# Kernel optimization log

Measured on AMD Instinct MI355X. Metric: run time of the kernel, lower is better.

## Reference

```python
import jax, jax.numpy as jnp
import numpy as np


def setup_inputs() -> dict:
    key = jax.random.key(0)
    ks = jax.random.split(key, 8)
    T, D = 8192, 36
    return {
        "embeddings": jax.random.normal(ks[0], (T, D), dtype=jnp.float32),
        "WQ_prog": jax.random.normal(ks[1], (2, D), dtype=jnp.float32),
        "WK_prog": jax.random.normal(ks[2], (2, D), dtype=jnp.float32),
        "WV_op": jax.random.normal(ks[3], (1, D), dtype=jnp.float32),
        "WV_arg": jax.random.normal(ks[4], (1, D), dtype=jnp.float32),
        "WQ_stack": jax.random.normal(ks[5], (2, D), dtype=jnp.float32),
        "WK_stack": jax.random.normal(ks[6], (2, D), dtype=jnp.float32),
        "WV_stack": jax.random.normal(ks[7], (1, D), dtype=jnp.float32),
    }


def reference(embeddings, WQ_prog, WK_prog, WV_op, WV_arg, WQ_stack, WK_stack, WV_stack):
    # --- program-fetch head: hard-argmax attention ---
    Q_prog = embeddings @ WQ_prog.T          # (T, 2)
    K_prog = embeddings @ WK_prog.T          # (T, 2)
    V_op = embeddings @ WV_op.T              # (T, 1)
    V_arg = embeddings @ WV_arg.T            # (T, 1)
    scores_prog = Q_prog @ K_prog.T          # (T, T)
    best_prog = jnp.argmax(scores_prog, axis=1)   # (T,)
    fetched_ops = V_op[best_prog, 0]
    fetched_args = V_arg[best_prog, 0]

    # --- stack-fetch head: hard-argmax attention ---
    Q_stack = embeddings @ WQ_stack.T        # (T, 2)
    K_stack = embeddings @ WK_stack.T        # (T, 2)
    V_stack = embeddings @ WV_stack.T        # (T, 1)
    scores_stack = Q_stack @ K_stack.T       # (T, T)
    best_stack = jnp.argmax(scores_stack, axis=1)
    fetched_vals = V_stack[best_stack, 0]

    return (fetched_ops, fetched_args, fetched_vals)
```

## Files before the change

### kernel.cpp

```cpp
#include <hip/hip_runtime.h>
#include <math.h>

#define T 8192
#define D 36
#define NCH 8
#define CHUNK (T / NCH)


__global__ __launch_bounds__(256) void proj_kernel(
    const float* __restrict__ E,
    const float* __restrict__ WQp, const float* __restrict__ WKp,
    const float* __restrict__ WVop, const float* __restrict__ WVarg,
    const float* __restrict__ WQs, const float* __restrict__ WKs,
    const float* __restrict__ WVs, float* __restrict__ ws) {
    int t = blockIdx.x * blockDim.x + threadIdx.x;
    if (t >= T) return;
    float e[D];
    const float4* Er = (const float4*)(E + t * D);
#pragma unroll
    for (int i = 0; i < D / 4; ++i) {
        float4 v = Er[i];
        e[4 * i + 0] = v.x; e[4 * i + 1] = v.y;
        e[4 * i + 2] = v.z; e[4 * i + 3] = v.w;
    }
    float qp0 = 0.f, qp1 = 0.f, kp0 = 0.f, kp1 = 0.f;
    float qs0 = 0.f, qs1 = 0.f, ks0 = 0.f, ks1 = 0.f;
    float vop = 0.f, varg = 0.f, vs = 0.f;
#pragma unroll
    for (int d = 0; d < D; ++d) {
        float ed = e[d];
        qp0 = fmaf(ed, WQp[d], qp0);
        qp1 = fmaf(ed, WQp[D + d], qp1);
        kp0 = fmaf(ed, WKp[d], kp0);
        kp1 = fmaf(ed, WKp[D + d], kp1);
        qs0 = fmaf(ed, WQs[d], qs0);
        qs1 = fmaf(ed, WQs[D + d], qs1);
        ks0 = fmaf(ed, WKs[d], ks0);
        ks1 = fmaf(ed, WKs[D + d], ks1);
        vop  = fmaf(ed, WVop[d], vop);
        varg = fmaf(ed, WVarg[d], varg);
        vs   = fmaf(ed, WVs[d], vs);
    }
    ws[t]          = qp0;
    ws[T + t]      = qp1;
    ws[2 * T + 2 * t]     = kp0;
    ws[2 * T + 2 * t + 1] = kp1;
    ws[4 * T + t]  = qs0;
    ws[5 * T + t]  = qs1;
    ws[6 * T + 2 * t]     = ks0;
    ws[6 * T + 2 * t + 1] = ks1;
    ws[8 * T + t]  = vop;
    ws[9 * T + t]  = varg;
    ws[10 * T + t] = vs;
}

__global__ __launch_bounds__(256) void argmax_kernel(
    const float* __restrict__ wsf, float* __restrict__ pv, int* __restrict__ pi) {
    const int head = blockIdx.z;
    const float* Q0 = wsf + (head ? 4 * T : 0);
    const float* Q1 = Q0 + T;
    const float2* K = (const float2*)(wsf + (head ? 6 * T : 2 * T));

    __shared__ float2 sk[CHUNK];
    const int j0 = blockIdx.y * CHUNK;
    for (int k = threadIdx.x; k < CHUNK; k += 256) sk[k] = K[j0 + k];
    __syncthreads();

    const int row = blockIdx.x * 256 + threadIdx.x;
    const float q0 = Q0[row], q1 = Q1[row];
    float best = -INFINITY;
    int bi = 0;
#pragma unroll 8
    for (int k = 0; k < CHUNK; ++k) {
        float2 kk = sk[k];
        float s = fmaf(q0, kk.x, q1 * kk.y);
        bool gt = s > best;
        best = gt ? s : best;
        bi   = gt ? k : bi;
    }
    const int prow = head * T + row;
    pv[prow * NCH + blockIdx.y] = best;
    pi[prow * NCH + blockIdx.y] = j0 + bi;
}

__global__ __launch_bounds__(256) void finalize_kernel(
    const float* __restrict__ wsf, const float* __restrict__ pv,
    const int* __restrict__ pi, float* __restrict__ out) {
    int idx = blockIdx.x * blockDim.x + threadIdx.x;
    if (idx >= 2 * T) return;
    const int head = idx >> 13;
    const int row  = idx & (T - 1);
    float best = -INFINITY;
    int bi = 0;
#pragma unroll
    for (int c = 0; c < NCH; ++c) {
        float v = pv[idx * NCH + c];
        int   i2 = pi[idx * NCH + c];
        bool gt = v > best;
        best = gt ? v : best;
        bi   = gt ? i2 : bi;
    }
    const float* Vop  = wsf + 8 * T;
    const float* Varg = wsf + 9 * T;
    const float* Vs   = wsf + 10 * T;
    if (head == 0) {
        out[row]     = Vop[bi];
        out[T + row] = Varg[bi];
    } else {
        out[2 * T + row] = Vs[bi];
    }
}

extern "C" void kernel_launch(void* const* d_in, const int* in_sizes, int n_in,
                              void* d_out, int out_size, void* d_ws, size_t ws_size,
                              hipStream_t stream) {
    const float* E     = (const float*)d_in[0];
    const float* WQp   = (const float*)d_in[1];
    const float* WKp   = (const float*)d_in[2];
    const float* WVop  = (const float*)d_in[3];
    const float* WVarg = (const float*)d_in[4];
    const float* WQs   = (const float*)d_in[5];
    const float* WKs   = (const float*)d_in[6];
    const float* WVs   = (const float*)d_in[7];
    float* out = (float*)d_out;

    float* wsf = (float*)d_ws;
    float* pv  = wsf + 11 * T;
    int*   pi  = (int*)(wsf + 11 * T + 2 * T * NCH);

    proj_kernel<<<T / 256, 256, 0, stream>>>(E, WQp, WKp, WVop, WVarg, WQs, WKs, WVs, wsf);

    dim3 gB(T / 256, NCH, 2);
    argmax_kernel<<<gB, 256, 0, stream>>>(wsf, pv, pi);

    finalize_kernel<<<(2 * T) / 256, 256, 0, stream>>>(wsf, pv, pi, out);
}
```

Baseline: 98.47 us.

## Fuse projection into argmax blocks and recompute values in finalize

Drops the separate projection kernel. Each argmax block now computes its key chunk and query directly from the embeddings, and the finalize kernel recomputes the value projection only for the selected row. The key-axis split goes from 8 to 16 chunks and the partial results are stored column-major for coalesced reads. This saves one launch and the workspace round-trip, at the cost of redundant key projection work in every row-block (32x per chunk) and extra embedding reads.

After: 99.37 us. About the same (+0.9%).

```diff
diff --git a/kernel.cpp b/kernel.cpp
--- a/kernel.cpp
+++ b/kernel.cpp
@@ -3,71 +3,63 @@
 
 #define T 8192
 #define D 36
-#define NCH 8
+#define NCH 16
 #define CHUNK (T / NCH)
+#define RPT (CHUNK / 256)
 
 
-__global__ __launch_bounds__(256) void proj_kernel(
-    const float* __restrict__ E,
-    const float* __restrict__ WQp, const float* __restrict__ WKp,
-    const float* __restrict__ WVop, const float* __restrict__ WVarg,
-    const float* __restrict__ WQs, const float* __restrict__ WKs,
-    const float* __restrict__ WVs, float* __restrict__ ws) {
-    int t = blockIdx.x * blockDim.x + threadIdx.x;
-    if (t >= T) return;
-    float e[D];
-    const float4* Er = (const float4*)(E + t * D);
+__device__ __forceinline__ void load_row(const float* __restrict__ E, int j,
+                                         float* e) {
+    const float4* Er = (const float4*)(E + j * D);
 #pragma unroll
     for (int i = 0; i < D / 4; ++i) {
         float4 v = Er[i];
-        e[4 * i + 0] = v.x; e[4 * i + 1] = v.y;
-        e[4 * i + 2] = v.z; e[4 * i + 3] = v.w;
+        e[4 * i + 0] = v.x;
+        e[4 * i + 1] = v.y;
+        e[4 * i + 2] = v.z;
+        e[4 * i + 3] = v.w;
     }
-    float qp0 = 0.f, qp1 = 0.f, kp0 = 0.f, kp1 = 0.f;
-    float qs0 = 0.f, qs1 = 0.f, ks0 = 0.f, ks1 = 0.f;
-    float vop = 0.f, varg = 0.f, vs = 0.f;
-#pragma unroll
-    for (int d = 0; d < D; ++d) {
-        float ed = e[d];
-        qp0 = fmaf(ed, WQp[d], qp0);
-        qp1 = fmaf(ed, WQp[D + d], qp1);
-        kp0 = fmaf(ed, WKp[d], kp0);
-        kp1 = fmaf(ed, WKp[D + d], kp1);
-        qs0 = fmaf(ed, WQs[d], qs0);
-        qs1 = fmaf(ed, WQs[D + d], qs1);
-        ks0 = fmaf(ed, WKs[d], ks0);
-        ks1 = fmaf(ed, WKs[D + d], ks1);
-        vop  = fmaf(ed, WVop[d], vop);
-        varg = fmaf(ed, WVarg[d], varg);
-        vs   = fmaf(ed, WVs[d], vs);
-    }
-    ws[t]          = qp0;
-    ws[T + t]      = qp1;
-    ws[2 * T + 2 * t]     = kp0;
-    ws[2 * T + 2 * t + 1] = kp1;
-    ws[4 * T + t]  = qs0;
-    ws[5 * T + t]  = qs1;
-    ws[6 * T + 2 * t]     = ks0;
-    ws[6 * T + 2 * t + 1] = ks1;
-    ws[8 * T + t]  = vop;
-    ws[9 * T + t]  = varg;
-    ws[10 * T + t] = vs;
 }
 
-__global__ __launch_bounds__(256) void argmax_kernel(
-    const float* __restrict__ wsf, float* __restrict__ pv, int* __restrict__ pi) {
+__global__ __launch_bounds__(256) void fused_proj_argmax(
+    const float* __restrict__ E,
+    const float* __restrict__ WQp, const float* __restrict__ WKp,
+    const float* __restrict__ WQs, const float* __restrict__ WKs,
+    float* __restrict__ pv, int* __restrict__ pi) {
     const int head = blockIdx.z;
-    const float* Q0 = wsf + (head ? 4 * T : 0);
-    const float* Q1 = Q0 + T;
-    const float2* K = (const float2*)(wsf + (head ? 6 * T : 2 * T));
+    const float* __restrict__ WQ = head ? WQs : WQp;
+    const float* __restrict__ WK = head ? WKs : WKp;
 
     __shared__ float2 sk[CHUNK];
     const int j0 = blockIdx.y * CHUNK;
-    for (int k = threadIdx.x; k < CHUNK; k += 256) sk[k] = K[j0 + k];
+
+#pragma unroll
+    for (int r = 0; r < RPT; ++r) {
+        const int j = j0 + r * 256 + threadIdx.x;
+        float e[D];
+        load_row(E, j, e);
+        float k0 = 0.f, k1 = 0.f;
+#pragma unroll
+        for (int d = 0; d < D; ++d) {
+            k0 = fmaf(e[d], WK[d], k0);
+            k1 = fmaf(e[d], WK[D + d], k1);
+        }
+        sk[r * 256 + threadIdx.x] = make_float2(k0, k1);
+    }
+
+    const int row = blockIdx.x * 256 + threadIdx.x;
+    float q0 = 0.f, q1 = 0.f;
+    {
+        float e[D];
+        load_row(E, row, e);
+#pragma unroll
+        for (int d = 0; d < D; ++d) {
+            q0 = fmaf(e[d], WQ[d], q0);
+            q1 = fmaf(e[d], WQ[D + d], q1);
+        }
+    }
     __syncthreads();
 
-    const int row = blockIdx.x * 256 + threadIdx.x;
-    const float q0 = Q0[row], q1 = Q1[row];
     float best = -INFINITY;
     int bi = 0;
 #pragma unroll 8
@@ -76,62 +68,73 @@
         float s = fmaf(q0, kk.x, q1 * kk.y);
         bool gt = s > best;
         best = gt ? s : best;
-        bi   = gt ? k : bi;
+        bi = gt ? k : bi;
     }
     const int prow = head * T + row;
-    pv[prow * NCH + blockIdx.y] = best;
-    pi[prow * NCH + blockIdx.y] = j0 + bi;
+    pv[blockIdx.y * 2 * T + prow] = best;
+    pi[blockIdx.y * 2 * T + prow] = j0 + bi;
 }
 
-__global__ __launch_bounds__(256) void finalize_kernel(
-    const float* __restrict__ wsf, const float* __restrict__ pv,
-    const int* __restrict__ pi, float* __restrict__ out) {
-    int idx = blockIdx.x * blockDim.x + threadIdx.x;
+__global__ __launch_bounds__(256) void finalize_fused(
+    const float* __restrict__ E,
+    const float* __restrict__ WVop, const float* __restrict__ WVarg,
+    const float* __restrict__ WVs,
+    const float* __restrict__ pv, const int* __restrict__ pi,
+    float* __restrict__ out) {
+    const int idx = blockIdx.x * blockDim.x + threadIdx.x;
     if (idx >= 2 * T) return;
     const int head = idx >> 13;
-    const int row  = idx & (T - 1);
+    const int row = idx & (T - 1);
+
     float best = -INFINITY;
     int bi = 0;
 #pragma unroll
     for (int c = 0; c < NCH; ++c) {
-        float v = pv[idx * NCH + c];
-        int   i2 = pi[idx * NCH + c];
+        float v = pv[c * 2 * T + idx];
+        int i2 = pi[c * 2 * T + idx];
         bool gt = v > best;
         best = gt ? v : best;
-        bi   = gt ? i2 : bi;
+        bi = gt ? i2 : bi;
     }
-    const float* Vop  = wsf + 8 * T;
-    const float* Varg = wsf + 9 * T;
-    const float* Vs   = wsf + 10 * T;
+
+    float e[D];
+    load_row(E, bi, e);
     if (head == 0) {
-        out[row]     = Vop[bi];
-        out[T + row] = Varg[bi];
+        float vop = 0.f, varg = 0.f;
+#pragma unroll
+        for (int d = 0; d < D; ++d) {
+            vop = fmaf(e[d], WVop[d], vop);
+            varg = fmaf(e[d], WVarg[d], varg);
+        }
+        out[row] = vop;
+        out[T + row] = varg;
     } else {
-        out[2 * T + row] = Vs[bi];
+        float vs = 0.f;
+#pragma unroll
+        for (int d = 0; d < D; ++d) vs = fmaf(e[d], WVs[d], vs);
+        out[2 * T + row] = vs;
     }
 }
 
 extern "C" void kernel_launch(void* const* d_in, const int* in_sizes, int n_in,
-                              void* d_out, int out_size, void* d_ws, size_t ws_size,
-                              hipStream_t stream) {
-    const float* E     = (const float*)d_in[0];
-    const float* WQp   = (const float*)d_in[1];
-    const float* WKp   = (const float*)d_in[2];
-    const float* WVop  = (const float*)d_in[3];
+                              void* d_out, int out_size, void* d_ws,
+                              size_t ws_size, hipStream_t stream) {
+    const float* E = (const float*)d_in[0];
+    const float* WQp = (const float*)d_in[1];
+    const float* WKp = (const float*)d_in[2];
+    const float* WVop = (const float*)d_in[3];
     const float* WVarg = (const float*)d_in[4];
-    const float* WQs   = (const float*)d_in[5];
-    const float* WKs   = (const float*)d_in[6];
-    const float* WVs   = (const float*)d_in[7];
+    const float* WQs = (const float*)d_in[5];
+    const float* WKs = (const float*)d_in[6];
+    const float* WVs = (const float*)d_in[7];
     float* out = (float*)d_out;
 
-    float* wsf = (float*)d_ws;
-    float* pv  = wsf + 11 * T;
-    int*   pi  = (int*)(wsf + 11 * T + 2 * T * NCH);
+    float* pv = (float*)d_ws;
+    int* pi = (int*)((float*)d_ws + 2 * T * NCH);
 
-    proj_kernel<<<T / 256, 256, 0, stream>>>(E, WQp, WKp, WVop, WVarg, WQs, WKs, WVs, wsf);
+    dim3 gA(T / 256, NCH, 2);
+    fused_proj_argmax<<<gA, 256, 0, stream>>>(E, WQp, WKp, WQs, WKs, pv, pi);
 
-    dim3 gB(T / 256, NCH, 2);
-    argmax_kernel<<<gB, 256, 0, stream>>>(wsf, pv, pi);
-
-    finalize_kernel<<<(2 * T) / 256, 256, 0, stream>>>(wsf, pv, pi, out);
+    finalize_fused<<<(2 * T) / 256, 256, 0, stream>>>(E, WVop, WVarg, WVs, pv,
+                                                      pi, out);
 }
```
